# Performance work log

Hardware: AMD Instinct MI355X
Metric: run time of the kernel (lower is better)

The kernel has to match this reference:

```python
import jax, jax.numpy as jnp
import numpy as np

H = 20  # attention heads


def setup_inputs() -> dict:
    key = jax.random.key(0)
    k1, k2, k3, k4 = jax.random.split(key, 4)
    d = 1280
    n_seq = 64
    seg_len = 2048
    T = n_seq * seg_len  # 131072 total ragged tokens
    c = 1  # single CLS query token
    embed = jax.random.normal(k1, (T, d), dtype=jnp.float32)
    cls = jax.random.normal(k2, (c, d), dtype=jnp.float32)
    # nn.Linear(embed_dim, embed_dim) params
    W_k = jax.random.normal(k3, (d, d), dtype=jnp.float32) / np.float32(np.sqrt(d))
    b_k = jax.random.normal(k4, (d,), dtype=jnp.float32) * 0.01
    # equal-length segments: cu_lens = [0, 2048, 4096, ..., 131072]
    cu_lens = (jnp.arange(n_seq + 1) * seg_len).astype(jnp.int32)
    return {"cls": cls, "embed": embed, "cu_lens": cu_lens, "max_len": seg_len,
            "W_k": W_k, "b_k": b_k}


def reference(cls, embed, cu_lens, max_len, W_k, b_k):
    # cls: (c, d), embed: (T, d), cu_lens: (n+1,) int32
    T, d = embed.shape
    c = cls.shape[0]
    n = cu_lens.shape[0] - 1
    dh = d // H

    # key projection (torch Linear: x @ W.T + b); value = raw embed (as in source)
    k = (embed @ W_k.T + b_k).reshape(T, H, dh)
    v = embed.reshape(T, H, dh)
    q = cls.reshape(c, H, dh)

    # segment id per token from cumulative lengths
    seg = jnp.searchsorted(cu_lens, jnp.arange(T, dtype=jnp.int32), side="right") - 1  # (T,)

    scale = np.float32(1.0 / np.sqrt(dh))  # flash-attn default softmax scale
    # scores without materializing repeated Q/K/V: (T, c, H)
    scores = jnp.einsum("chd,thd->tch", q, k) * scale

    # segment-wise numerically-stable softmax over tokens, then weighted-V sum
    m = jax.ops.segment_max(scores, seg, num_segments=n)            # (n, c, H)
    p = jnp.exp(scores - m[seg])                                    # (T, c, H)
    denom = jax.ops.segment_sum(p, seg, num_segments=n)             # (n, c, H)
    num = jax.ops.segment_sum(p[..., None] * v[:, None, :, :], seg,
                              num_segments=n)                       # (n, c, H, dh)
    out = num / denom[..., None]                                    # (n, c, H, dh)
    return out.reshape(n, c, d)
```

## Files before the change

### kernel.cpp

```cpp
#include <hip/hip_runtime.h>

#define H 20
#define D 1280
#define DH 64
#define TB1 128
#define DCH 32
#define LSTR 33
#define TB2 256

__global__ __launch_bounds__(256) void prep_u(const float* __restrict__ cls,
                                              const float* __restrict__ Wk,
                                              const float* __restrict__ bk,
                                              float* __restrict__ uT,
                                              float* __restrict__ qb) {
  const float scale = 0.125f;
  const int bph = D / 256;
  const int h = blockIdx.x / bph;
  const int j = (blockIdx.x % bph) * 256 + threadIdx.x;
  float s = 0.f;
  #pragma unroll 8
  for (int i = 0; i < DH; ++i)
    s += cls[h * DH + i] * Wk[(long)(h * DH + i) * D + j];
  uT[j * H + h] = s * scale;
  if (blockIdx.x == 0 && threadIdx.x < H) {
    const int hh = threadIdx.x;
    float b = 0.f;
    for (int i = 0; i < DH; ++i) b += cls[hh * DH + i] * bk[hh * DH + i];
    qb[hh] = b * scale;
  }
}

__global__ __launch_bounds__(256) void scores_k(const float* __restrict__ embed,
                                                const float* __restrict__ uT,
                                                const float* __restrict__ qb,
                                                float* __restrict__ p_g) {
  __shared__ float tile[TB1 * LSTR];
  const int tid = threadIdx.x;
  const long tb = (long)blockIdx.x * TB1;
  float acc[H];
  #pragma unroll
  for (int h = 0; h < H; ++h) acc[h] = 0.f;

  const int srow = tid >> 3;
  const int scol = (tid & 7) * 4;
  const int tokl = tid & (TB1 - 1);
  const int jhalf = __builtin_amdgcn_readfirstlane(tid >> 7);

  for (int c = 0; c < D / DCH; ++c) {
    const int jc = c * DCH;
    #pragma unroll
    for (int r = 0; r < 4; ++r) {
      const int row = srow + r * 32;
      const float4 v = *reinterpret_cast<const float4*>(&embed[(tb + row) * D + jc + scol]);
      float* w = &tile[row * LSTR + scol];
      w[0] = v.x; w[1] = v.y; w[2] = v.z; w[3] = v.w;
    }
    __syncthreads();
    float x[DCH / 2];
    #pragma unroll
    for (int q = 0; q < DCH / 2; ++q)
      x[q] = tile[tokl * LSTR + jhalf * (DCH / 2) + q];
    #pragma unroll
    for (int q = 0; q < DCH / 2; ++q) {
      const float* u = &uT[(jc + jhalf * (DCH / 2) + q) * H];
      #pragma unroll
      for (int h = 0; h < H; ++h) acc[h] += x[q] * u[h];
    }
    __syncthreads();
  }

  float* scratch = tile;
  if (jhalf) {
    #pragma unroll
    for (int h = 0; h < H; ++h) scratch[tokl * H + h] = acc[h];
  }
  __syncthreads();
  if (!jhalf) {
    float o[H];
    #pragma unroll
    for (int h = 0; h < H; ++h)
      o[h] = __expf(acc[h] + scratch[tokl * H + h] + qb[h]);
    float4* pp = reinterpret_cast<float4*>(&p_g[(tb + tokl) * H]);
    #pragma unroll
    for (int k = 0; k < 5; ++k)
      pp[k] = make_float4(o[4 * k], o[4 * k + 1], o[4 * k + 2], o[4 * k + 3]);
  }
}

__global__ __launch_bounds__(320) void accum_k(const float* __restrict__ embed,
                                               const float* __restrict__ p_g,
                                               float* __restrict__ num_g) {
  const int tid = threadIdx.x;
  const long tb = (long)blockIdx.x * TB2;
  const int h = tid >> 4;
  float4 acc = make_float4(0.f, 0.f, 0.f, 0.f);
  const float4* e4 = reinterpret_cast<const float4*>(embed);
  #pragma unroll 4
  for (int tt = 0; tt < TB2; ++tt) {
    const long t = tb + tt;
    const float pv = p_g[t * H + h];
    const float4 x = e4[t * (D / 4) + tid];
    acc.x += pv * x.x; acc.y += pv * x.y; acc.z += pv * x.z; acc.w += pv * x.w;
  }
  reinterpret_cast<float4*>(num_g)[(long)blockIdx.x * (D / 4) + tid] = acc;
}

__global__ __launch_bounds__(256) void combine_k(const float* __restrict__ p_g,
                                                 const float* __restrict__ num_g,
                                                 float* __restrict__ out,
                                                 int seg_len) {
  __shared__ float wpart[4 * H];
  __shared__ float den_s[H];
  const int tid = threadIdx.x;
  const long base = (long)blockIdx.x * seg_len;
  float dp[H];
  #pragma unroll
  for (int h = 0; h < H; ++h) dp[h] = 0.f;
  const float4* p4 = reinterpret_cast<const float4*>(p_g);
  const int kiters = seg_len >> 8;
  for (int k = 0; k < kiters; ++k) {
    const long t = base + tid + (k << 8);
    const long r = t * (H / 4);
    const float4 a = p4[r], b = p4[r + 1], c = p4[r + 2], d2 = p4[r + 3], e = p4[r + 4];
    dp[0] += a.x;  dp[1] += a.y;  dp[2] += a.z;  dp[3] += a.w;
    dp[4] += b.x;  dp[5] += b.y;  dp[6] += b.z;  dp[7] += b.w;
    dp[8] += c.x;  dp[9] += c.y;  dp[10] += c.z; dp[11] += c.w;
    dp[12] += d2.x; dp[13] += d2.y; dp[14] += d2.z; dp[15] += d2.w;
    dp[16] += e.x; dp[17] += e.y;  dp[18] += e.z; dp[19] += e.w;
  }
  #pragma unroll
  for (int off = 32; off >= 1; off >>= 1) {
    #pragma unroll
    for (int h = 0; h < H; ++h) dp[h] += __shfl_xor(dp[h], off, 64);
  }
  const int lane = tid & 63, w = tid >> 6;
  if (lane == 0) {
    #pragma unroll
    for (int h = 0; h < H; ++h) wpart[w * H + h] = dp[h];
  }
  __syncthreads();
  if (tid < H)
    den_s[tid] = wpart[tid] + wpart[H + tid] + wpart[2 * H + tid] + wpart[3 * H + tid];
  __syncthreads();
  const int nb0 = (int)(base / TB2);
  const int nsplit = seg_len / TB2;
  #pragma unroll
  for (int r5 = 0; r5 < 5; ++r5) {
    const int d = tid + 256 * r5;
    float s = 0.f;
    for (int k = 0; k < nsplit; ++k)
      s += num_g[(long)(nb0 + k) * D + d];
    out[(long)blockIdx.x * D + d] = s / den_s[d >> 6];
  }
}

extern "C" void kernel_launch(void* const* d_in, const int* in_sizes, int n_in,
                              void* d_out, int out_size, void* d_ws, size_t ws_size,
                              hipStream_t stream) {
  const float* cls   = (const float*)d_in[0];
  const float* embed = (const float*)d_in[1];
  const float* Wk    = (const float*)d_in[4];
  const float* bk    = (const float*)d_in[5];
  float* out = (float*)d_out;

  const int dmodel = in_sizes[0];
  const long T = in_sizes[1] / dmodel;
  const int n = in_sizes[2] - 1;
  const int seg_len = (int)(T / n);

  char* ws = (char*)d_ws;
  float* uT  = (float*)(ws);
  float* qb  = (float*)(ws + 102400);
  float* p   = (float*)(ws + 131072);
  float* num = (float*)(ws + 131072 + (size_t)T * H * 4);

  prep_u<<<(dmodel / 256) * H, 256, 0, stream>>>(cls, Wk, bk, uT, qb);
  scores_k<<<(int)(T / TB1), 256, 0, stream>>>(embed, uT, qb, p);
  accum_k<<<(int)(T / TB2), 320, 0, stream>>>(embed, p, num);
  combine_k<<<n, 256, 0, stream>>>(p, num, out, seg_len);
}
```

Before: 295.7 us.

## Fuse score and weighted-value accumulation into one pass over embed

New measurement: 444.8 us. 50.4% more time.

```diff
diff --git a/kernel.cpp b/kernel.cpp
--- a/kernel.cpp
+++ b/kernel.cpp
@@ -3,10 +3,12 @@
 #define H 20
 #define D 1280
 #define DH 64
-#define TB1 128
-#define DCH 32
-#define LSTR 33
-#define TB2 256
+#define NT 8
+#define TSTR 1288
+#define BPS 8
+#define NTH 320
+#define NW 5
+#define NCH (D / 40)
 
 __global__ __launch_bounds__(256) void prep_u(const float* __restrict__ cls,
                                               const float* __restrict__ Wk,
@@ -30,127 +32,131 @@
   }
 }
 
-__global__ __launch_bounds__(256) void scores_k(const float* __restrict__ embed,
-                                                const float* __restrict__ uT,
-                                                const float* __restrict__ qb,
-                                                float* __restrict__ p_g) {
-  __shared__ float tile[TB1 * LSTR];
+__global__ __launch_bounds__(NTH, 4) void fused_k(const float* __restrict__ embed,
+                                                  const float* __restrict__ uT,
+                                                  const float* __restrict__ qb,
+                                                  float* __restrict__ num_g,
+                                                  float* __restrict__ den_g,
+                                                  int seg_len) {
+  __shared__ float tile[NT * TSTR];
+  __shared__ float red[NW * NT * H];
+  __shared__ float p_s[NT * H];
   const int tid = threadIdx.x;
-  const long tb = (long)blockIdx.x * TB1;
-  float acc[H];
-  #pragma unroll
-  for (int h = 0; h < H; ++h) acc[h] = 0.f;
+  const int lane = tid & 63;
+  const int wv = tid >> 6;
+  const int tt = lane & (NT - 1);
+  const int q = lane >> 3;
+  const int jl = wv * 8 + q;
+  const int seg = blockIdx.x / BPS;
+  const int sub = blockIdx.x % BPS;
+  const int tpb = seg_len / BPS;
+  const long tok0 = (long)seg * seg_len + (long)sub * tpb;
+  const int nst = tpb / NT;
+  const float4* e4 = (const float4*)embed;
+  const float4* u4 = (const float4*)uT;
 
-  const int srow = tid >> 3;
-  const int scol = (tid & 7) * 4;
-  const int tokl = tid & (TB1 - 1);
-  const int jhalf = __builtin_amdgcn_readfirstlane(tid >> 7);
+  float4 nacc = make_float4(0.f, 0.f, 0.f, 0.f);
+  float den_acc = 0.f;
 
-  for (int c = 0; c < D / DCH; ++c) {
-    const int jc = c * DCH;
-    #pragma unroll
-    for (int r = 0; r < 4; ++r) {
-      const int row = srow + r * 32;
-      const float4 v = *reinterpret_cast<const float4*>(&embed[(tb + row) * D + jc + scol]);
-      float* w = &tile[row * LSTR + scol];
-      w[0] = v.x; w[1] = v.y; w[2] = v.z; w[3] = v.w;
+  float4 s0, s1, s2, s3, s4, s5, s6, s7;
+  {
+    const long rb = tok0 * (D / 4) + tid;
+    s0 = e4[rb];        s1 = e4[rb + 320];  s2 = e4[rb + 640];  s3 = e4[rb + 960];
+    s4 = e4[rb + 1280]; s5 = e4[rb + 1600]; s6 = e4[rb + 1920]; s7 = e4[rb + 2240];
+  }
+
+  for (int st = 0; st < nst; ++st) {
+    __syncthreads();
+    const int tw = tid << 2;
+    *(float4*)&tile[0 * TSTR + tw] = s0;  *(float4*)&tile[1 * TSTR + tw] = s1;
+    *(float4*)&tile[2 * TSTR + tw] = s2;  *(float4*)&tile[3 * TSTR + tw] = s3;
+    *(float4*)&tile[4 * TSTR + tw] = s4;  *(float4*)&tile[5 * TSTR + tw] = s5;
+    *(float4*)&tile[6 * TSTR + tw] = s6;  *(float4*)&tile[7 * TSTR + tw] = s7;
+    if (st + 1 < nst) {
+      const long rb = (tok0 + (long)(st + 1) * NT) * (D / 4) + tid;
+      s0 = e4[rb];        s1 = e4[rb + 320];  s2 = e4[rb + 640];  s3 = e4[rb + 960];
+      s4 = e4[rb + 1280]; s5 = e4[rb + 1600]; s6 = e4[rb + 1920]; s7 = e4[rb + 2240];
     }
     __syncthreads();
-    float x[DCH / 2];
+
+    float acc[H];
     #pragma unroll
-    for (int q = 0; q < DCH / 2; ++q)
-      x[q] = tile[tokl * LSTR + jhalf * (DCH / 2) + q];
+    for (int h = 0; h < H; ++h) acc[h] = 0.f;
+    #pragma unroll 2
+    for (int c = 0; c < NCH; ++c) {
+      const int j = c * 40 + jl;
+      const float x = tile[tt * TSTR + j];
+      const int j5 = j * 5;
+      const float4 b0 = u4[j5], b1 = u4[j5 + 1], b2 = u4[j5 + 2],
+                   b3 = u4[j5 + 3], b4 = u4[j5 + 4];
+      acc[0]  += x * b0.x; acc[1]  += x * b0.y; acc[2]  += x * b0.z; acc[3]  += x * b0.w;
+      acc[4]  += x * b1.x; acc[5]  += x * b1.y; acc[6]  += x * b1.z; acc[7]  += x * b1.w;
+      acc[8]  += x * b2.x; acc[9]  += x * b2.y; acc[10] += x * b2.z; acc[11] += x * b2.w;
+      acc[12] += x * b3.x; acc[13] += x * b3.y; acc[14] += x * b3.z; acc[15] += x * b3.w;
+      acc[16] += x * b4.x; acc[17] += x * b4.y; acc[18] += x * b4.z; acc[19] += x * b4.w;
+    }
     #pragma unroll
-    for (int q = 0; q < DCH / 2; ++q) {
-      const float* u = &uT[(jc + jhalf * (DCH / 2) + q) * H];
+    for (int h = 0; h < H; ++h) {
+      float v = acc[h];
+      v += __shfl_xor(v, 8, 64);
+      v += __shfl_xor(v, 16, 64);
+      v += __shfl_xor(v, 32, 64);
+      acc[h] = v;
+    }
+    if (lane < NT) {
       #pragma unroll
-      for (int h = 0; h < H; ++h) acc[h] += x[q] * u[h];
+      for (int h = 0; h < H; ++h) red[(wv * NT + lane) * H + h] = acc[h];
     }
     __syncthreads();
+    if (tid < NT * H) {
+      const int h2 = tid % H;
+      float s = red[tid] + red[NT * H + tid] + red[2 * NT * H + tid] +
+                red[3 * NT * H + tid] + red[4 * NT * H + tid];
+      p_s[tid] = __expf(s + qb[h2]);
+    }
+    __syncthreads();
+
+    float pv[NT];
+    #pragma unroll
+    for (int k = 0; k < NT; ++k) pv[k] = p_s[k * H + (tid >> 4)];
+    #pragma unroll
+    for (int k = 0; k < NT; ++k) {
+      const float4 x4 = *(const float4*)&tile[k * TSTR + tw];
+      nacc.x += pv[k] * x4.x; nacc.y += pv[k] * x4.y;
+      nacc.z += pv[k] * x4.z; nacc.w += pv[k] * x4.w;
+    }
+    if (tid < H) {
+      float dsum = 0.f;
+      #pragma unroll
+      for (int k = 0; k < NT; ++k) dsum += p_s[k * H + tid];
+      den_acc += dsum;
+    }
   }
 
-  float* scratch = tile;
-  if (jhalf) {
+  ((float4*)num_g)[(long)blockIdx.x * (D / 4) + tid] = nacc;
+  if (tid < H) den_g[blockIdx.x * H + tid] = den_acc;
+}
+
+__global__ __launch_bounds__(256) void combine2(const float* __restrict__ num_g,
+                                                const float* __restrict__ den_g,
+                                                float* __restrict__ out) {
+  __shared__ float den_s[H];
+  const int tid = threadIdx.x;
+  const int seg = blockIdx.x;
+  if (tid < H) {
+    float s = 0.f;
     #pragma unroll
-    for (int h = 0; h < H; ++h) scratch[tokl * H + h] = acc[h];
+    for (int b = 0; b < BPS; ++b) s += den_g[(seg * BPS + b) * H + tid];
+    den_s[tid] = s;
   }
   __syncthreads();
-  if (!jhalf) {
-    float o[H];
+  #pragma unroll
+  for (int r = 0; r < D / 256; ++r) {
+    const int d = r * 256 + tid;
+    float s = 0.f;
     #pragma unroll
-    for (int h = 0; h < H; ++h)
-      o[h] = __expf(acc[h] + scratch[tokl * H + h] + qb[h]);
-    float4* pp = reinterpret_cast<float4*>(&p_g[(tb + tokl) * H]);
-    #pragma unroll
-    for (int k = 0; k < 5; ++k)
-      pp[k] = make_float4(o[4 * k], o[4 * k + 1], o[4 * k + 2], o[4 * k + 3]);
-  }
-}
-
-__global__ __launch_bounds__(320) void accum_k(const float* __restrict__ embed,
-                                               const float* __restrict__ p_g,
-                                               float* __restrict__ num_g) {
-  const int tid = threadIdx.x;
-  const long tb = (long)blockIdx.x * TB2;
-  const int h = tid >> 4;
-  float4 acc = make_float4(0.f, 0.f, 0.f, 0.f);
-  const float4* e4 = reinterpret_cast<const float4*>(embed);
-  #pragma unroll 4
-  for (int tt = 0; tt < TB2; ++tt) {
-    const long t = tb + tt;
-    const float pv = p_g[t * H + h];
-    const float4 x = e4[t * (D / 4) + tid];
-    acc.x += pv * x.x; acc.y += pv * x.y; acc.z += pv * x.z; acc.w += pv * x.w;
-  }
-  reinterpret_cast<float4*>(num_g)[(long)blockIdx.x * (D / 4) + tid] = acc;
-}
-
-__global__ __launch_bounds__(256) void combine_k(const float* __restrict__ p_g,
-                                                 const float* __restrict__ num_g,
-                                                 float* __restrict__ out,
-                                                 int seg_len) {
-  __shared__ float wpart[4 * H];
-  __shared__ float den_s[H];
-  const int tid = threadIdx.x;
-  const long base = (long)blockIdx.x * seg_len;
-  float dp[H];
-  #pragma unroll
-  for (int h = 0; h < H; ++h) dp[h] = 0.f;
-  const float4* p4 = reinterpret_cast<const float4*>(p_g);
-  const int kiters = seg_len >> 8;
-  for (int k = 0; k < kiters; ++k) {
-    const long t = base + tid + (k << 8);
-    const long r = t * (H / 4);
-    const float4 a = p4[r], b = p4[r + 1], c = p4[r + 2], d2 = p4[r + 3], e = p4[r + 4];
-    dp[0] += a.x;  dp[1] += a.y;  dp[2] += a.z;  dp[3] += a.w;
-    dp[4] += b.x;  dp[5] += b.y;  dp[6] += b.z;  dp[7] += b.w;
-    dp[8] += c.x;  dp[9] += c.y;  dp[10] += c.z; dp[11] += c.w;
-    dp[12] += d2.x; dp[13] += d2.y; dp[14] += d2.z; dp[15] += d2.w;
-    dp[16] += e.x; dp[17] += e.y;  dp[18] += e.z; dp[19] += e.w;
-  }
-  #pragma unroll
-  for (int off = 32; off >= 1; off >>= 1) {
-    #pragma unroll
-    for (int h = 0; h < H; ++h) dp[h] += __shfl_xor(dp[h], off, 64);
-  }
-  const int lane = tid & 63, w = tid >> 6;
-  if (lane == 0) {
-    #pragma unroll
-    for (int h = 0; h < H; ++h) wpart[w * H + h] = dp[h];
-  }
-  __syncthreads();
-  if (tid < H)
-    den_s[tid] = wpart[tid] + wpart[H + tid] + wpart[2 * H + tid] + wpart[3 * H + tid];
-  __syncthreads();
-  const int nb0 = (int)(base / TB2);
-  const int nsplit = seg_len / TB2;
-  #pragma unroll
-  for (int r5 = 0; r5 < 5; ++r5) {
-    const int d = tid + 256 * r5;
-    float s = 0.f;
-    for (int k = 0; k < nsplit; ++k)
-      s += num_g[(long)(nb0 + k) * D + d];
-    out[(long)blockIdx.x * D + d] = s / den_s[d >> 6];
+    for (int b = 0; b < BPS; ++b) s += num_g[(long)(seg * BPS + b) * D + d];
+    out[(long)seg * D + d] = s / den_s[d >> 6];
   }
 }
 
@@ -168,14 +174,15 @@
   const int n = in_sizes[2] - 1;
   const int seg_len = (int)(T / n);
 
+  const int nblk = n * BPS;
+
   char* ws = (char*)d_ws;
   float* uT  = (float*)(ws);
   float* qb  = (float*)(ws + 102400);
-  float* p   = (float*)(ws + 131072);
-  float* num = (float*)(ws + 131072 + (size_t)T * H * 4);
+  float* num = (float*)(ws + 131072);
+  float* den = (float*)(ws + 131072 + (size_t)nblk * D * 4);
 
   prep_u<<<(dmodel / 256) * H, 256, 0, stream>>>(cls, Wk, bk, uT, qb);
-  scores_k<<<(int)(T / TB1), 256, 0, stream>>>(embed, uT, qb, p);
-  accum_k<<<(int)(T / TB2), 320, 0, stream>>>(embed, p, num);
-  combine_k<<<n, 256, 0, stream>>>(p, num, out, seg_len);
+  fused_k<<<nblk, NTH, 0, stream>>>(embed, uT, qb, num, den, seg_len);
+  combine2<<<n, 256, 0, stream>>>(num, den, out);
 }
```
